# Kernel tuning notes

Hardware: AMD Instinct MI355X
Metric: run time of the kernel (lower is better)

## Reference

```python
import jax, jax.numpy as jnp
import numpy as np

BETA = 1.0

def setup_inputs() -> dict:
    key = jax.random.key(0)
    k1, k2, k3 = jax.random.split(key, 3)
    B, T, G, D, V = 4, 2048, 8, 128, 1024
    inputs = jax.random.normal(k1, (B, T, G * D), dtype=jnp.float32)
    paddings = jax.random.randint(k2, (B, T), 0, 2, dtype=jnp.int32)
    codebook = jax.random.normal(k3, (V, G, D), dtype=jnp.float32)  # (V, G, D)
    return {"inputs": inputs, "paddings": paddings, "codebook": codebook}

def reference(inputs, paddings, codebook):
    B, T, _ = inputs.shape
    V, G, D = codebook.shape
    sg = jax.lax.stop_gradient
    x = inputs.reshape(B, T, G, D)
    x2 = jnp.sum(x * x, axis=-1)                      # (B,T,G)
    c2 = jnp.sum(codebook * codebook, axis=-1)        # (V,G)
    xc = jnp.einsum('btgd,vgd->btvg', x, codebook)    # (B,T,V,G) GEMM
    dist = x2[:, :, None, :] - 2.0 * xc + c2[None, None]
    ids = jnp.argmin(dist, axis=2)                    # (B,T,G) int
    # gather codebook[ids[b,t,g], g] -> (B,T,G,D)
    quantized = codebook[ids, jnp.arange(G)[None, None, :]]
    mask = (1 - paddings).astype(jnp.float32)[:, :, None, None]  # (B,T,1,1)
    msum = mask.sum()
    kmeans_loss = jnp.sum(((quantized - sg(x)) ** 2) * mask) / msum
    commitment_loss = jnp.sum(((x - sg(quantized)) ** 2) * mask) / msum
    total_loss = kmeans_loss + BETA * commitment_loss
    quantized_st = ((x + sg(quantized - x)) * mask).reshape(B, T, G * D)
    ids = jnp.where((paddings == 1)[:, :, None], -1, ids.astype(jnp.int32))
    return (ids, quantized_st, kmeans_loss, commitment_loss, total_loss)
```

## Files before the change

### kernel.cpp

```cpp
#include <hip/hip_runtime.h>
#include <math.h>

typedef _Float16 f16;
typedef f16 half8 __attribute__((ext_vector_type(8)));
typedef float f32x4 __attribute__((ext_vector_type(4)));

#define BT 8192
#define NG 8
#define ND 128
#define NV 1024
#define MARGIN  0.08f
#define MARGIN3 0.16f
#define BM 64
#define BN 64
#define NT 16
#define FULLBIT 0x40000000u

#define OUT_IDS 0
#define OUT_Q   65536
#define OUT_L   (65536 + 8388608)

#define OFF_C2A    0
#define OFF_C2B    8192
#define OFF_LOSSG  81920
#define OFF_CNT    147456
#define OFF_FLAGS  147464
#define OFF_CBH    213000
#define OFF_PART   (OFF_CBH + 524288)
#define OFF_CAND2  (OFF_PART + 64)
#define OFF_TOKMAP (OFF_CAND2 + 65536)

__device__ __forceinline__ void gll16(const f16* g, f16* l) {
    __builtin_amdgcn_global_load_lds(
        (const __attribute__((address_space(1))) unsigned int*)g,
        (__attribute__((address_space(3))) unsigned int*)l, 16, 0, 0);
}

__global__ __launch_bounds__(256) void compact_kernel(
    const int* __restrict__ pad, int* __restrict__ cnt,
    int* __restrict__ tokmap) {
    __shared__ int ps[256];
    const int tid = threadIdx.x;
    const int base = tid * 32;
    int c = 0;
#pragma unroll
    for (int i = 0; i < 32; ++i) c += 1 - pad[base + i];
    ps[tid] = c;
    __syncthreads();
    for (int st = 1; st < 256; st <<= 1) {
        int v = (tid >= st) ? ps[tid - st] : 0;
        __syncthreads();
        ps[tid] += v;
        __syncthreads();
    }
    int o = ps[tid] - c;
    if (tid == 255) {
        cnt[1] = ps[255];
        cnt[0] = 0;
    }
    for (int i = 0; i < 32; ++i) {
        int tok = base + i;
        if (!pad[tok]) tokmap[o++] = tok;
    }
}

__global__ __launch_bounds__(256) void prep_kernel(
    const float* __restrict__ cb, f16* __restrict__ cbh,
    float* __restrict__ c2a, float* __restrict__ c2b) {
    __shared__ float prod[16][16][9];
    __shared__ float rbuf[16][8];
    const int tid = threadIdx.x;
    const int rloc = tid >> 4, t = tid & 15;
    const int idx = blockIdx.x * 16 + rloc;
    const int v = idx >> 3, g = idx & 7;
    const int rl = v & 63;
    const float4* row4 = (const float4*)(cb + (size_t)idx * ND);

    float4 a = row4[t * 2], b = row4[t * 2 + 1];
    float vv[8] = {a.x, a.y, a.z, a.w, b.x, b.y, b.z, b.w};
    half8 h;
#pragma unroll
    for (int e = 0; e < 8; ++e) {
        prod[rloc][t][e] = __fmul_rn(vv[e], vv[e]);
        h[e] = (f16)vv[e];
    }
    int cn = v >> 6;
    size_t base = ((size_t)(g * 16 + cn)) * 8192 + rl * 128;
    *(half8*)(cbh + base + ((t ^ (rl & 7)) * 8)) = h;
    __syncthreads();

    if (t < 8) {
        float r = 0.f;
#pragma unroll
        for (int tt = 0; tt < 16; ++tt)
            r = __fadd_rn(r, prod[rloc][tt][t]);
        rbuf[rloc][t] = r;
    }
    __syncthreads();
    if (t == 0) {
        float s = __fadd_rn(
            __fadd_rn(__fadd_rn(rbuf[rloc][0], rbuf[rloc][1]),
                      __fadd_rn(rbuf[rloc][2], rbuf[rloc][3])),
            __fadd_rn(__fadd_rn(rbuf[rloc][4], rbuf[rloc][5]),
                      __fadd_rn(rbuf[rloc][6], rbuf[rloc][7])));
        c2a[idx] = s;
        c2b[g * NV + v] = s;
    }
}

__global__ __launch_bounds__(256) void padfill(
    const int* __restrict__ pad, float* __restrict__ out_ids,
    float* __restrict__ out_q, float* __restrict__ lossg) {
    const int gt = blockIdx.x * 256 + threadIdx.x;
    const float4 z = make_float4(0.f, 0.f, 0.f, 0.f);
#pragma unroll 4
    for (int i = gt; i < BT * NG * ND / 4; i += 512 * 256) {
        int tok = i >> 8;
        if (pad[tok]) ((float4*)out_q)[i] = z;
    }
    if (gt < BT * NG) {
        int tok = gt >> 3;
        if (pad[tok]) {
            out_ids[gt] = -1.0f;
            lossg[gt] = 0.0f;
        }
    }
}

__global__ __launch_bounds__(256, 4) void mfma_gemm(
    const float* __restrict__ x, const f16* __restrict__ cbh,
    const float* __restrict__ cb, const float* __restrict__ c2b,
    const int* __restrict__ ncnt, const int* __restrict__ tokmap,
    float* __restrict__ out_ids, float* __restrict__ out_q,
    float* __restrict__ lossg, int* __restrict__ cnt,
    int* __restrict__ flags, int* __restrict__ cand2) {
    __shared__ __align__(16) f16 Bh[2][BN * ND];
    __shared__ __align__(16) float c2s[NV];
    __shared__ int idsL[BM];
    __shared__ int tokL[BM];

    const int tid = threadIdx.x;
    const int b = blockIdx.x;
    const int g = b & 7;
    const int count = *ncnt;
    const int tile_base = (b >> 3) * BM;
    if (tile_base >= count) return;
    const int lane = tid & 63;
    const int w = tid >> 6;
    const int wr = w & 1, wc = w >> 1;
    const int l15 = lane & 15, l4 = lane >> 4;

    ((float4*)c2s)[tid] = ((const float4*)(c2b + (size_t)g * NV))[tid];
    {
        const f16* sh = cbh + ((size_t)(g * 16 + 0)) * 8192;
#pragma unroll
        for (int it = 0; it < 4; ++it)
            gll16(sh + it * 2048 + tid * 8, &Bh[0][it * 2048 + tid * 8]);
    }

    int tokA_[2];
#pragma unroll
    for (int ti = 0; ti < 2; ++ti) {
        int slot = tile_base + wr * 32 + ti * 16 + l15;
        tokA_[ti] = tokmap[(slot < count) ? slot : 0];
    }

    half8 ah[4][2];
#pragma unroll
    for (int kk = 0; kk < 4; ++kk)
#pragma unroll
        for (int ti = 0; ti < 2; ++ti) {
            const float* ap = x + ((size_t)tokA_[ti] * NG + g) * ND
                              + kk * 32 + l4 * 8;
            float4 p0 = *(const float4*)ap, p1 = *(const float4*)(ap + 4);
            float vv[8] = {p0.x, p0.y, p0.z, p0.w, p1.x, p1.y, p1.z, p1.w};
            half8 h;
#pragma unroll
            for (int j = 0; j < 8; ++j) h[j] = (f16)vv[j];
            ah[kk][ti] = h;
        }

    float d1s[2][4], d2s[2][4], d3s[2][4];
    int id1s[2][4], id2s[2][4];
#pragma unroll
    for (int ti = 0; ti < 2; ++ti)
#pragma unroll
        for (int r = 0; r < 4; ++r) {
            d1s[ti][r] = INFINITY;
            d2s[ti][r] = INFINITY;
            d3s[ti][r] = INFINITY;
            id1s[ti][r] = 0;
            id2s[ti][r] = 0;
        }

    int buf = 0;
#pragma unroll 1
    for (int t = 0; t < NT; ++t) {
        asm volatile("s_waitcnt vmcnt(0) lgkmcnt(0)" ::: "memory");
        __builtin_amdgcn_s_barrier();
        __builtin_amdgcn_sched_barrier(0);

        if (t + 1 < NT) {
            const f16* sh = cbh + ((size_t)(g * 16 + t + 1)) * 8192;
#pragma unroll
            for (int it = 0; it < 4; ++it)
                gll16(sh + it * 2048 + tid * 8,
                      &Bh[buf ^ 1][it * 2048 + tid * 8]);
        }

        f32x4 acc[2][2];
#pragma unroll
        for (int ti = 0; ti < 2; ++ti)
#pragma unroll
            for (int tj = 0; tj < 2; ++tj)
                acc[ti][tj] = (f32x4){0.f, 0.f, 0.f, 0.f};

#pragma unroll
        for (int kk = 0; kk < 4; ++kk) {
            half8 bh[2];
#pragma unroll
            for (int tj = 0; tj < 2; ++tj) {
                int rw = wc * 32 + tj * 16 + l15;
                bh[tj] = *(const half8*)(
                    &Bh[buf][rw * 128 + (((kk * 4 + l4) ^ (rw & 7)) << 3)]);
            }
#pragma unroll
            for (int ti = 0; ti < 2; ++ti)
#pragma unroll
                for (int tj = 0; tj < 2; ++tj)
                    acc[ti][tj] = __builtin_amdgcn_mfma_f32_16x16x32_f16(
                        ah[kk][ti], bh[tj], acc[ti][tj], 0, 0, 0);
        }

#pragma unroll
        for (int tj = 0; tj < 2; ++tj) {
            int code = t * BN + wc * 32 + tj * 16 + l15;
            float c2v = c2s[code];
#pragma unroll
            for (int ti = 0; ti < 2; ++ti)
#pragma unroll
                for (int r = 0; r < 4; ++r) {
                    float dv = fmaf(-2.0f, acc[ti][tj][r], c2v);
                    bool lt1 = dv < d1s[ti][r];
                    bool lt2 = dv < d2s[ti][r];
                    bool lt3 = dv < d3s[ti][r];
                    d3s[ti][r] = lt2 ? d2s[ti][r] : (lt3 ? dv : d3s[ti][r]);
                    d2s[ti][r] = lt1 ? d1s[ti][r] : (lt2 ? dv : d2s[ti][r]);
                    id2s[ti][r] = lt1 ? id1s[ti][r] : (lt2 ? code : id2s[ti][r]);
                    d1s[ti][r] = lt1 ? dv : d1s[ti][r];
                    id1s[ti][r] = lt1 ? code : id1s[ti][r];
                }
        }
        buf ^= 1;
    }

    __syncthreads();
    float4* red = (float4*)&Bh[0][0];
    float* redd3 = (float*)(red + 128);
#pragma unroll
    for (int ti = 0; ti < 2; ++ti)
#pragma unroll
        for (int r = 0; r < 4; ++r) {
            float d1 = d1s[ti][r], d2 = d2s[ti][r], d3 = d3s[ti][r];
            int i1 = id1s[ti][r], i2 = id2s[ti][r];
#pragma unroll
            for (int m = 1; m < 16; m <<= 1) {
                float od1 = __shfl_xor(d1, m);
                float od2 = __shfl_xor(d2, m);
                float od3 = __shfl_xor(d3, m);
                int oi1 = __shfl_xor(i1, m);
                int oi2 = __shfl_xor(i2, m);
                bool ow = od1 < d1;
                float w1 = ow ? od1 : d1, w2 = ow ? od2 : d2, w3 = ow ? od3 : d3;
                int wi1 = ow ? oi1 : i1, wi2 = ow ? oi2 : i2;
                float l1 = ow ? d1 : od1, l2 = ow ? d2 : od2;
                int li1 = ow ? i1 : oi1;
                d1 = w1; i1 = wi1;
                bool t2 = w2 < l1;
                d2 = t2 ? w2 : l1;
                i2 = t2 ? wi2 : li1;
                d3 = t2 ? fminf(w3, l1) : fminf(w2, l2);
            }
            if (l15 == 0) {
                int o = wc * BM + wr * 32 + ti * 16 + l4 * 4 + r;
                red[o] = make_float4(d1, __int_as_float(i1), d2,
                                     __int_as_float(i2));
                redd3[o] = d3;
            }
        }
    __syncthreads();

    if (tid < BM) {
        float4 A = red[tid], C = red[BM + tid];
        float a3 = redd3[tid], c3 = redd3[BM + tid];
        float a1 = A.x, a2 = A.z, c1 = C.x, c2q = C.z;
        int ai1 = __float_as_int(A.y), ai2 = __float_as_int(A.w);
        int ci1 = __float_as_int(C.y), ci2 = __float_as_int(C.w);
        bool cw = c1 < a1;
        float w1 = cw ? c1 : a1, w2 = cw ? c2q : a2, w3 = cw ? c3 : a3;
        int wi1 = cw ? ci1 : ai1, wi2 = cw ? ci2 : ai2;
        float l1 = cw ? a1 : c1, l2 = cw ? a2 : c2q;
        int li1 = cw ? ai1 : ci1;
        float d1 = w1;
        int i1 = wi1;
        bool t2 = w2 < l1;
        float d2 = t2 ? w2 : l1;
        int i2 = t2 ? wi2 : li1;
        float d3 = t2 ? fminf(w3, l1) : fminf(w2, l2);

        int slot = tile_base + tid;
        if (slot < count) {
            int tok = tokmap[slot];
            int idx = tok * NG + g;
            out_ids[idx] = (float)i1;
            idsL[tid] = i1;
            tokL[tid] = tok;
            if (d2 - d1 < MARGIN) {
                int pos = atomicAdd(cnt, 1);
                flags[pos] = idx;
                cand2[idx] = i2 | ((d3 - d1 < MARGIN3) ? (int)FULLBIT : 0);
            }
        } else {
            idsL[tid] = -1;
        }
    }
    __syncthreads();

#pragma unroll
    for (int it = 0; it < 8; ++it) {
        int i = it * 256 + tid;
        int tl = i >> 5, d4 = i & 31;
        int id = idsL[tl];
        if (id >= 0) {
            int tok = tokL[tl];
            size_t rowo = ((size_t)tok * NG + g) * ND;
            float4 q = ((const float4*)(cb + ((size_t)id * NG + g) * ND))[d4];
            float4 a = ((const float4*)(x + rowo))[d4];
            float e0 = q.x - a.x, e1 = q.y - a.y;
            float e2 = q.z - a.z, e3 = q.w - a.w;
            float s = e0 * e0 + e1 * e1 + e2 * e2 + e3 * e3;
            ((float4*)(out_q + rowo))[d4] = q;
#pragma unroll
            for (int m = 1; m < 32; m <<= 1) s += __shfl_xor(s, m);
            if (d4 == 0) lossg[tok * NG + g] = s;
        }
    }
}

__global__ __launch_bounds__(256) void recheck(
    const float* __restrict__ x, const float* __restrict__ cb,
    const float* __restrict__ c2w, const int* __restrict__ cnt,
    const int* __restrict__ flags, const int* __restrict__ cand2,
    float* __restrict__ out_ids, float* __restrict__ out_q,
    float* __restrict__ lossg) {
    __shared__ __align__(16) float xs[ND];
    __shared__ float2 redw[4];
    __shared__ int bidS;
    const int tid = threadIdx.x;
    const int lane = tid & 63;
    const int w = tid >> 6;
    const int n_f = cnt[0];

    for (int f = blockIdx.x * 4 + w; f < n_f; f += gridDim.x * 4) {
        int idx = flags[f];
        unsigned cc = (unsigned)cand2[idx];
        if (cc & FULLBIT) continue;
        int g = idx & 7;
        int id1 = (int)out_ids[idx];
        int id2 = (int)(cc & ~FULLBIT);
        float2 xv = ((const float2*)(x + (size_t)idx * ND))[lane];
        float2 av = ((const float2*)(cb + ((size_t)id1 * NG + g) * ND))[lane];
        float2 bv = ((const float2*)(cb + ((size_t)id2 * NG + g) * ND))[lane];
        float eA0 = xv.x - av.x, eA1 = xv.y - av.y;
        float eB0 = xv.x - bv.x, eB1 = xv.y - bv.y;
        float sA = eA0 * eA0 + eA1 * eA1;
        float sB = eB0 * eB0 + eB1 * eB1;
#pragma unroll
        for (int m = 1; m < 64; m <<= 1) {
            sA += __shfl_xor(sA, m);
            sB += __shfl_xor(sB, m);
        }
        int win;
        float sw;
        if (sA < sB) { win = id1; sw = sA; }
        else if (sB < sA) { win = id2; sw = sB; }
        else { win = (id1 < id2) ? id1 : id2; sw = sA; }
        if (win != id1) {
            if (lane == 0) {
                out_ids[idx] = (float)win;
                lossg[idx] = sw;
            }
            if (lane < 32) {
                float4 q = ((const float4*)(cb + ((size_t)win * NG + g) * ND))[lane];
                ((float4*)(out_q + (size_t)idx * ND))[lane] = q;
            }
        }
    }
    __syncthreads();

    for (int f = blockIdx.x; f < n_f; f += gridDim.x) {
        int idx = flags[f];
        if (!(((unsigned)cand2[idx]) & FULLBIT)) continue;
        int g = idx & 7;
        __syncthreads();
        if (tid < 32)
            ((float4*)xs)[tid] = ((const float4*)(x + (size_t)idx * ND))[tid];
        __syncthreads();

        float rr[8];
#pragma unroll
        for (int j = 0; j < 8; ++j) rr[j] = 0.0f;
#pragma unroll
        for (int i = 0; i < 32; ++i) {
            float4 v = ((const float4*)xs)[i];
            int j0 = (i * 4) & 7;
            rr[j0 + 0] = __fadd_rn(rr[j0 + 0], __fmul_rn(v.x, v.x));
            rr[j0 + 1] = __fadd_rn(rr[j0 + 1], __fmul_rn(v.y, v.y));
            rr[j0 + 2] = __fadd_rn(rr[j0 + 2], __fmul_rn(v.z, v.z));
            rr[j0 + 3] = __fadd_rn(rr[j0 + 3], __fmul_rn(v.w, v.w));
        }
        float x2v = __fadd_rn(
            __fadd_rn(__fadd_rn(rr[0], rr[1]), __fadd_rn(rr[2], rr[3])),
            __fadd_rn(__fadd_rn(rr[4], rr[5]), __fadd_rn(rr[6], rr[7])));

        float best = INFINITY;
        int bid = 0x7FFFFFFF;
        float s0 = 0.f, s1 = 0.f, s2 = 0.f, s3 = 0.f;
#pragma unroll
        for (int i = 0; i < 32; ++i) {
            float4 a = ((const float4*)xs)[i];
            float4 q0 = ((const float4*)(cb + ((size_t)(tid) * NG + g) * ND))[i];
            float4 q1 = ((const float4*)(cb + ((size_t)(tid + 256) * NG + g) * ND))[i];
            float4 q2 = ((const float4*)(cb + ((size_t)(tid + 512) * NG + g) * ND))[i];
            float4 q3 = ((const float4*)(cb + ((size_t)(tid + 768) * NG + g) * ND))[i];
            s0 = fmaf(a.x, q0.x, s0); s0 = fmaf(a.y, q0.y, s0);
            s0 = fmaf(a.z, q0.z, s0); s0 = fmaf(a.w, q0.w, s0);
            s1 = fmaf(a.x, q1.x, s1); s1 = fmaf(a.y, q1.y, s1);
            s1 = fmaf(a.z, q1.z, s1); s1 = fmaf(a.w, q1.w, s1);
            s2 = fmaf(a.x, q2.x, s2); s2 = fmaf(a.y, q2.y, s2);
            s2 = fmaf(a.z, q2.z, s2); s2 = fmaf(a.w, q2.w, s2);
            s3 = fmaf(a.x, q3.x, s3); s3 = fmaf(a.y, q3.y, s3);
            s3 = fmaf(a.z, q3.z, s3); s3 = fmaf(a.w, q3.w, s3);
        }
        float dd[4] = {s0, s1, s2, s3};
#pragma unroll
        for (int jj = 0; jj < 4; ++jj) {
            int c = tid + 256 * jj;
            float d = __fadd_rn(__fsub_rn(x2v, __fmul_rn(2.0f, dd[jj])),
                                c2w[(size_t)c * NG + g]);
            if (d < best || (d == best && c < bid)) { best = d; bid = c; }
        }
#pragma unroll
        for (int m = 1; m < 64; m <<= 1) {
            float od = __shfl_xor(best, m);
            int ob = __shfl_xor(bid, m);
            if (od < best || (od == best && ob < bid)) { best = od; bid = ob; }
        }
        if (lane == 0) redw[w] = make_float2(best, __int_as_float(bid));
        __syncthreads();
        if (tid == 0) {
            float b2 = redw[0].x;
            int i2 = __float_as_int(redw[0].y);
#pragma unroll
            for (int ww = 1; ww < 4; ++ww) {
                float ob = redw[ww].x;
                int oi = __float_as_int(redw[ww].y);
                if (ob < b2 || (ob == b2 && oi < i2)) { b2 = ob; i2 = oi; }
            }
            out_ids[idx] = (float)i2;
            bidS = i2;
        }
        __syncthreads();
        if (tid < 32) {
            float4 q = ((const float4*)(cb + ((size_t)bidS * NG + g) * ND))[tid];
            ((float4*)(out_q + (size_t)idx * ND))[tid] = q;
            float4 a = ((const float4*)xs)[tid];
            float e0 = q.x - a.x, e1 = q.y - a.y;
            float e2 = q.z - a.z, e3 = q.w - a.w;
            float s = e0 * e0 + e1 * e1 + e2 * e2 + e3 * e3;
#pragma unroll
            for (int m = 1; m < 32; m <<= 1) s += __shfl_xor(s, m);
            if (tid == 0) lossg[idx] = s;
        }
    }
}

__global__ __launch_bounds__(256) void loss_part(
    const float* __restrict__ lossg, float* __restrict__ part) {
    __shared__ float sr[256];
    const int tid = threadIdx.x;
    float4 v = ((const float4*)lossg)[blockIdx.x * 256 + tid];
    sr[tid] = ((v.x + v.y) + (v.z + v.w));
    __syncthreads();
    for (int st = 128; st > 0; st >>= 1) {
        if (tid < st) sr[tid] += sr[tid + st];
        __syncthreads();
    }
    if (tid == 0) part[blockIdx.x] = sr[0];
}

__global__ __launch_bounds__(256) void final_kernel(
    const int* __restrict__ pad, const float* __restrict__ part,
    float* __restrict__ out_l) {
    __shared__ int mr[256];
    const int tid = threadIdx.x;
    int m = 0;
#pragma unroll
    for (int i = 0; i < 32; ++i) m += 1 - pad[tid * 32 + i];
    mr[tid] = m;
    __syncthreads();
    for (int st = 128; st > 0; st >>= 1) {
        if (tid < st) mr[tid] += mr[tid + st];
        __syncthreads();
    }
    if (tid == 0) {
        float s = 0.f;
#pragma unroll
        for (int i = 0; i < 64; ++i) s += part[i];
        float k = s / (float)mr[0];
        out_l[0] = k;
        out_l[1] = k;
        out_l[2] = k + k;
    }
}

extern "C" void kernel_launch(void* const* d_in, const int* in_sizes, int n_in,
                              void* d_out, int out_size, void* d_ws, size_t ws_size,
                              hipStream_t stream) {
    const float* x = (const float*)d_in[0];
    const int* pad = (const int*)d_in[1];
    const float* cb = (const float*)d_in[2];
    float* out = (float*)d_out;
    float* ws = (float*)d_ws;

    float* ws_c2a = ws + OFF_C2A;
    float* ws_c2b = ws + OFF_C2B;
    float* ws_lossg = ws + OFF_LOSSG;
    int* ws_cnt = (int*)(ws + OFF_CNT);
    int* ws_flags = (int*)(ws + OFF_FLAGS);
    f16* cbh = (f16*)(ws + OFF_CBH);
    float* ws_part = ws + OFF_PART;
    int* ws_cand2 = (int*)(ws + OFF_CAND2);
    int* ws_tokmap = (int*)(ws + OFF_TOKMAP);

    compact_kernel<<<1, 256, 0, stream>>>(pad, ws_cnt, ws_tokmap);
    prep_kernel<<<NV * NG / 16, 256, 0, stream>>>(cb, cbh, ws_c2a, ws_c2b);
    padfill<<<512, 256, 0, stream>>>(pad, out + OUT_IDS, out + OUT_Q, ws_lossg);
    mfma_gemm<<<(BT / BM) * NG, 256, 0, stream>>>(x, cbh, cb, ws_c2b,
                                                  ws_cnt + 1, ws_tokmap,
                                                  out + OUT_IDS, out + OUT_Q,
                                                  ws_lossg, ws_cnt, ws_flags,
                                                  ws_cand2);
    recheck<<<512, 256, 0, stream>>>(x, cb, ws_c2a, ws_cnt, ws_flags,
                                     ws_cand2, out + OUT_IDS, out + OUT_Q,
                                     ws_lossg);
    loss_part<<<64, 256, 0, stream>>>(ws_lossg, ws_part);
    final_kernel<<<1, 256, 0, stream>>>(pad, ws_part, out + OUT_L);
}
```

Measured before the change: 83.09 us.

## Split codebook search across two blocks per tile and merge in separate kernel

The GEMM grid is doubled so each block searches half the codebook (NT 16→8). Each block writes its top-3 partial distances and ids to workspace, and a new merge kernel combines the two halves, writes ids and quantized rows, and flags near-ties. The compaction kernel is folded into prep_kernel as an extra block, and final_kernel reuses the count instead of re-reducing paddings. The aim is more parallelism and fewer launches, in exchange for an extra kernel and round trips of the partial results through global memory.

```diff
diff --git a/kernel.cpp b/kernel.cpp
--- a/kernel.cpp
+++ b/kernel.cpp
@@ -13,7 +13,7 @@
 #define MARGIN3 0.16f
 #define BM 64
 #define BN 64
-#define NT 16
+#define NT 8
 #define FULLBIT 0x40000000u
 
 #define OUT_IDS 0
@@ -29,6 +29,8 @@
 #define OFF_PART   (OFF_CBH + 524288)
 #define OFF_CAND2  (OFF_PART + 64)
 #define OFF_TOKMAP (OFF_CAND2 + 65536)
+#define OFF_P4     (OFF_TOKMAP + 8192)
+#define OFF_P1     (OFF_P4 + 524288)
 
 __device__ __forceinline__ void gll16(const f16* g, f16* l) {
     __builtin_amdgcn_global_load_lds(
@@ -36,40 +38,39 @@
         (__attribute__((address_space(3))) unsigned int*)l, 16, 0, 0);
 }
 
-__global__ __launch_bounds__(256) void compact_kernel(
-    const int* __restrict__ pad, int* __restrict__ cnt,
-    int* __restrict__ tokmap) {
-    __shared__ int ps[256];
+__global__ __launch_bounds__(256) void prep_kernel(
+    const float* __restrict__ cb, const int* __restrict__ pad,
+    f16* __restrict__ cbh, float* __restrict__ c2a, float* __restrict__ c2b,
+    int* __restrict__ cnt, int* __restrict__ tokmap) {
     const int tid = threadIdx.x;
-    const int base = tid * 32;
-    int c = 0;
-#pragma unroll
-    for (int i = 0; i < 32; ++i) c += 1 - pad[base + i];
-    ps[tid] = c;
-    __syncthreads();
-    for (int st = 1; st < 256; st <<= 1) {
-        int v = (tid >= st) ? ps[tid - st] : 0;
+    if (blockIdx.x == 512) {
+        __shared__ int ps[256];
+        const int base = tid * 32;
+        int c = 0;
+#pragma unroll
+        for (int i = 0; i < 32; ++i) c += 1 - pad[base + i];
+        ps[tid] = c;
         __syncthreads();
-        ps[tid] += v;
-        __syncthreads();
-    }
-    int o = ps[tid] - c;
-    if (tid == 255) {
-        cnt[1] = ps[255];
-        cnt[0] = 0;
-    }
-    for (int i = 0; i < 32; ++i) {
-        int tok = base + i;
-        if (!pad[tok]) tokmap[o++] = tok;
-    }
-}
-
-__global__ __launch_bounds__(256) void prep_kernel(
-    const float* __restrict__ cb, f16* __restrict__ cbh,
-    float* __restrict__ c2a, float* __restrict__ c2b) {
+        for (int st = 1; st < 256; st <<= 1) {
+            int v = (tid >= st) ? ps[tid - st] : 0;
+            __syncthreads();
+            ps[tid] += v;
+            __syncthreads();
+        }
+        int o = ps[tid] - c;
+        if (tid == 255) {
+            cnt[1] = ps[255];
+            cnt[0] = 0;
+        }
+        for (int i = 0; i < 32; ++i) {
+            int tok = base + i;
+            if (!pad[tok]) tokmap[o++] = tok;
+        }
+        return;
+    }
+
     __shared__ float prod[16][16][9];
     __shared__ float rbuf[16][8];
-    const int tid = threadIdx.x;
     const int rloc = tid >> 4, t = tid & 15;
     const int idx = blockIdx.x * 16 + rloc;
     const int v = idx >> 3, g = idx & 7;
@@ -129,21 +130,18 @@
 
 __global__ __launch_bounds__(256, 4) void mfma_gemm(
     const float* __restrict__ x, const f16* __restrict__ cbh,
-    const float* __restrict__ cb, const float* __restrict__ c2b,
-    const int* __restrict__ ncnt, const int* __restrict__ tokmap,
-    float* __restrict__ out_ids, float* __restrict__ out_q,
-    float* __restrict__ lossg, int* __restrict__ cnt,
-    int* __restrict__ flags, int* __restrict__ cand2) {
+    const float* __restrict__ c2b, const int* __restrict__ ncnt,
+    const int* __restrict__ tokmap, float4* __restrict__ part4,
+    float* __restrict__ part1) {
     __shared__ __align__(16) f16 Bh[2][BN * ND];
     __shared__ __align__(16) float c2s[NV];
-    __shared__ int idsL[BM];
-    __shared__ int tokL[BM];
 
     const int tid = threadIdx.x;
     const int b = blockIdx.x;
-    const int g = b & 7;
+    const int h = b & 1;
+    const int g = (b >> 1) & 7;
     const int count = *ncnt;
-    const int tile_base = (b >> 3) * BM;
+    const int tile_base = (b >> 4) * BM;
     if (tile_base >= count) return;
     const int lane = tid & 63;
     const int w = tid >> 6;
@@ -152,7 +150,7 @@
 
     ((float4*)c2s)[tid] = ((const float4*)(c2b + (size_t)g * NV))[tid];
     {
-        const f16* sh = cbh + ((size_t)(g * 16 + 0)) * 8192;
+        const f16* sh = cbh + ((size_t)(g * 16 + h * 8)) * 8192;
 #pragma unroll
         for (int it = 0; it < 4; ++it)
             gll16(sh + it * 2048 + tid * 8, &Bh[0][it * 2048 + tid * 8]);
@@ -174,10 +172,10 @@
                               + kk * 32 + l4 * 8;
             float4 p0 = *(const float4*)ap, p1 = *(const float4*)(ap + 4);
             float vv[8] = {p0.x, p0.y, p0.z, p0.w, p1.x, p1.y, p1.z, p1.w};
-            half8 h;
-#pragma unroll
-            for (int j = 0; j < 8; ++j) h[j] = (f16)vv[j];
-            ah[kk][ti] = h;
+            half8 hh;
+#pragma unroll
+            for (int j = 0; j < 8; ++j) hh[j] = (f16)vv[j];
+            ah[kk][ti] = hh;
         }
 
     float d1s[2][4], d2s[2][4], d3s[2][4];
@@ -201,7 +199,7 @@
         __builtin_amdgcn_sched_barrier(0);
 
         if (t + 1 < NT) {
-            const f16* sh = cbh + ((size_t)(g * 16 + t + 1)) * 8192;
+            const f16* sh = cbh + ((size_t)(g * 16 + h * 8 + t + 1)) * 8192;
 #pragma unroll
             for (int it = 0; it < 4; ++it)
                 gll16(sh + it * 2048 + tid * 8,
@@ -234,7 +232,7 @@
 
 #pragma unroll
         for (int tj = 0; tj < 2; ++tj) {
-            int code = t * BN + wc * 32 + tj * 16 + l15;
+            int code = h * 512 + t * BN + wc * 32 + tj * 16 + l15;
             float c2v = c2s[code];
 #pragma unroll
             for (int ti = 0; ti < 2; ++ti)
@@ -293,14 +291,12 @@
     if (tid < BM) {
         float4 A = red[tid], C = red[BM + tid];
         float a3 = redd3[tid], c3 = redd3[BM + tid];
-        float a1 = A.x, a2 = A.z, c1 = C.x, c2q = C.z;
-        int ai1 = __float_as_int(A.y), ai2 = __float_as_int(A.w);
-        int ci1 = __float_as_int(C.y), ci2 = __float_as_int(C.w);
-        bool cw = c1 < a1;
-        float w1 = cw ? c1 : a1, w2 = cw ? c2q : a2, w3 = cw ? c3 : a3;
-        int wi1 = cw ? ci1 : ai1, wi2 = cw ? ci2 : ai2;
-        float l1 = cw ? a1 : c1, l2 = cw ? a2 : c2q;
-        int li1 = cw ? ai1 : ci1;
+        bool cw = C.x < A.x;
+        float w1 = cw ? C.x : A.x, w2 = cw ? C.z : A.z, w3 = cw ? c3 : a3;
+        int wi1 = cw ? __float_as_int(C.y) : __float_as_int(A.y);
+        int wi2 = cw ? __float_as_int(C.w) : __float_as_int(A.w);
+        float l1 = cw ? A.x : C.x, l2 = cw ? A.z : C.z;
+        int li1 = cw ? __float_as_int(A.y) : __float_as_int(C.y);
         float d1 = w1;
         int i1 = wi1;
         bool t2 = w2 < l1;
@@ -310,31 +306,74 @@
 
         int slot = tile_base + tid;
         if (slot < count) {
-            int tok = tokmap[slot];
-            int idx = tok * NG + g;
-            out_ids[idx] = (float)i1;
-            idsL[tid] = i1;
-            tokL[tid] = tok;
-            if (d2 - d1 < MARGIN) {
-                int pos = atomicAdd(cnt, 1);
-                flags[pos] = idx;
-                cand2[idx] = i2 | ((d3 - d1 < MARGIN3) ? (int)FULLBIT : 0);
-            }
-        } else {
-            idsL[tid] = -1;
-        }
-    }
-    __syncthreads();
-
-#pragma unroll
-    for (int it = 0; it < 8; ++it) {
+            int o = slot * 16 + g * 2 + h;
+            part4[o] = make_float4(d1, __int_as_float(i1), d2,
+                                   __int_as_float(i2));
+            part1[o] = d3;
+        }
+    }
+}
+
+__global__ __launch_bounds__(256) void merge_kernel(
+    const float* __restrict__ x, const float* __restrict__ cb,
+    const int* __restrict__ ncnt, const int* __restrict__ tokmap,
+    const float4* __restrict__ part4, const float* __restrict__ part1,
+    float* __restrict__ out_ids, float* __restrict__ out_q,
+    float* __restrict__ lossg, int* __restrict__ cnt,
+    int* __restrict__ flags, int* __restrict__ cand2) {
+    __shared__ int idsM[256];
+    __shared__ int tokM[32];
+    const int tid = threadIdx.x;
+    const int count = *ncnt;
+    const int sbase = blockIdx.x * 32;
+    if (sbase >= count) return;
+    const int sl = tid >> 3, g = tid & 7;
+    const int slot = sbase + sl;
+
+    if (tid < 32)
+        tokM[tid] = (sbase + tid < count) ? tokmap[sbase + tid] : -1;
+
+    if (slot < count) {
+        int o0 = slot * 16 + g * 2;
+        float4 A = part4[o0], C = part4[o0 + 1];
+        float a3 = part1[o0], c3 = part1[o0 + 1];
+        bool cw = C.x < A.x;
+        float w1 = cw ? C.x : A.x, w2 = cw ? C.z : A.z, w3 = cw ? c3 : a3;
+        int wi1 = cw ? __float_as_int(C.y) : __float_as_int(A.y);
+        int wi2 = cw ? __float_as_int(C.w) : __float_as_int(A.w);
+        float l1 = cw ? A.x : C.x, l2 = cw ? A.z : C.z;
+        int li1 = cw ? __float_as_int(A.y) : __float_as_int(C.y);
+        float d1 = w1;
+        int i1 = wi1;
+        bool t2 = w2 < l1;
+        float d2 = t2 ? w2 : l1;
+        int i2 = t2 ? wi2 : li1;
+        float d3 = t2 ? fminf(w3, l1) : fminf(w2, l2);
+
+        int tok = tokmap[slot];
+        int idx = tok * NG + g;
+        out_ids[idx] = (float)i1;
+        idsM[tid] = i1;
+        if (d2 - d1 < MARGIN) {
+            int pos = atomicAdd(cnt, 1);
+            flags[pos] = idx;
+            cand2[idx] = i2 | ((d3 - d1 < MARGIN3) ? (int)FULLBIT : 0);
+        }
+    } else {
+        idsM[tid] = -1;
+    }
+    __syncthreads();
+
+#pragma unroll 1
+    for (int it = 0; it < 32; ++it) {
         int i = it * 256 + tid;
-        int tl = i >> 5, d4 = i & 31;
-        int id = idsL[tl];
+        int r = i >> 5, d4 = i & 31;
+        int id = idsM[r];
         if (id >= 0) {
-            int tok = tokL[tl];
-            size_t rowo = ((size_t)tok * NG + g) * ND;
-            float4 q = ((const float4*)(cb + ((size_t)id * NG + g) * ND))[d4];
+            int tok = tokM[r >> 3];
+            int gg = r & 7;
+            size_t rowo = ((size_t)tok * NG + gg) * ND;
+            float4 q = ((const float4*)(cb + ((size_t)id * NG + gg) * ND))[d4];
             float4 a = ((const float4*)(x + rowo))[d4];
             float e0 = q.x - a.x, e1 = q.y - a.y;
             float e2 = q.z - a.z, e3 = q.w - a.w;
@@ -342,7 +381,7 @@
             ((float4*)(out_q + rowo))[d4] = q;
 #pragma unroll
             for (int m = 1; m < 32; m <<= 1) s += __shfl_xor(s, m);
-            if (d4 == 0) lossg[tok * NG + g] = s;
+            if (d4 == 0) lossg[tok * NG + gg] = s;
         }
     }
 }
@@ -499,25 +538,15 @@
     if (tid == 0) part[blockIdx.x] = sr[0];
 }
 
-__global__ __launch_bounds__(256) void final_kernel(
-    const int* __restrict__ pad, const float* __restrict__ part,
+__global__ __launch_bounds__(64) void final_kernel(
+    const int* __restrict__ cnt, const float* __restrict__ part,
     float* __restrict__ out_l) {
-    __shared__ int mr[256];
     const int tid = threadIdx.x;
-    int m = 0;
-#pragma unroll
-    for (int i = 0; i < 32; ++i) m += 1 - pad[tid * 32 + i];
-    mr[tid] = m;
-    __syncthreads();
-    for (int st = 128; st > 0; st >>= 1) {
-        if (tid < st) mr[tid] += mr[tid + st];
-        __syncthreads();
-    }
+    float s = part[tid];
+#pragma unroll
+    for (int m = 1; m < 64; m <<= 1) s += __shfl_xor(s, m);
     if (tid == 0) {
-        float s = 0.f;
-#pragma unroll
-        for (int i = 0; i < 64; ++i) s += part[i];
-        float k = s / (float)mr[0];
+        float k = s / (float)cnt[1];
         out_l[0] = k;
         out_l[1] = k;
         out_l[2] = k + k;
@@ -542,18 +571,22 @@
     float* ws_part = ws + OFF_PART;
     int* ws_cand2 = (int*)(ws + OFF_CAND2);
     int* ws_tokmap = (int*)(ws + OFF_TOKMAP);
-
-    compact_kernel<<<1, 256, 0, stream>>>(pad, ws_cnt, ws_tokmap);
-    prep_kernel<<<NV * NG / 16, 256, 0, stream>>>(cb, cbh, ws_c2a, ws_c2b);
+    float4* ws_p4 = (float4*)(ws + OFF_P4);
+    float* ws_p1 = ws + OFF_P1;
+
+    prep_kernel<<<513, 256, 0, stream>>>(cb, pad, cbh, ws_c2a, ws_c2b,
+                                         ws_cnt, ws_tokmap);
     padfill<<<512, 256, 0, stream>>>(pad, out + OUT_IDS, out + OUT_Q, ws_lossg);
-    mfma_gemm<<<(BT / BM) * NG, 256, 0, stream>>>(x, cbh, cb, ws_c2b,
-                                                  ws_cnt + 1, ws_tokmap,
-                                                  out + OUT_IDS, out + OUT_Q,
-                                                  ws_lossg, ws_cnt, ws_flags,
-                                                  ws_cand2);
+    mfma_gemm<<<(BT / BM) * NG * 2, 256, 0, stream>>>(x, cbh, ws_c2b,
+                                                      ws_cnt + 1, ws_tokmap,
+                                                      ws_p4, ws_p1);
+    merge_kernel<<<256, 256, 0, stream>>>(x, cb, ws_cnt + 1, ws_tokmap,
+                                          ws_p4, ws_p1, out + OUT_IDS,
+                                          out + OUT_Q, ws_lossg, ws_cnt,
+                                          ws_flags, ws_cand2);
     recheck<<<512, 256, 0, stream>>>(x, cb, ws_c2a, ws_cnt, ws_flags,
                                      ws_cand2, out + OUT_IDS, out + OUT_Q,
                                      ws_lossg);
     loss_part<<<64, 256, 0, stream>>>(ws_lossg, ws_part);
-    final_kernel<<<1, 256, 0, stream>>>(pad, ws_part, out + OUT_L);
-}
+    final_kernel<<<1, 64, 0, stream>>>(ws_cnt, ws_part, out + OUT_L);
+}
```

New measurement: 100.8 us. 1.21x slower.
